# Kernel optimization log

Hardware: AMD Instinct MI355X
Metric: run time of the kernel (lower is better)

## Reference

```python
import jax, jax.numpy as jnp
import numpy as np
from jax import lax

LBDA = 0.5   # soft-min temperature from OTAM_cum_dist_v2 default
EPS = 0.01   # cos_sim epsilon


def otam_cum_dist(dists, lbda=LBDA):
    """Soft-DTW-style OTAM DP. dists: [nq, ns, L, S] -> [nq, ns].
    Faithful to OTAM_cum_dist_v2: pad last dim by (1,1) with zeros, then run the
    row-wise recurrence. Soft-min computed via stable logsumexp (same math as
    -lbda*log(sum exp(-x/lbda)))."""
    nq, ns, L, S = dists.shape
    d = jnp.pad(dists, ((0, 0), (0, 0), (0, 0), (1, 1)))  # [nq, ns, L, W], W=S+2
    W = S + 2
    # Row 0: cum[0, m] = cum[0, m-1] + d[0, m], cum[0, 0] = 0
    row0 = jnp.concatenate(
        [jnp.zeros((nq, ns, 1), d.dtype), jnp.cumsum(d[:, :, 0, 1:], axis=-1)], axis=-1)
    if L == 1:
        return row0[..., -1]

    m_idx = jnp.arange(1, W)
    include_up = (m_idx == 1) | (m_idx == W - 1)  # only first/last cols use cum[l-1, m]
    INF = jnp.asarray(jnp.inf, d.dtype)

    def row_step(prev_row, d_row):
        # prev_row, d_row: [nq, ns, W]
        xs = (
            jnp.moveaxis(d_row[:, :, 1:], -1, 0),        # d[l, m],       [W-1, nq, ns]
            jnp.moveaxis(prev_row[:, :, :-1], -1, 0),    # cum[l-1, m-1]
            jnp.moveaxis(prev_row[:, :, 1:], -1, 0),     # cum[l-1, m]
            include_up,
        )

        def col_step(cur_left, x):
            d_m, p_diag, p_up, inc = x
            up = jnp.where(inc, p_up, INF)               # masked term -> exp(-inf)=0
            terms = jnp.stack([p_diag, cur_left, up])    # [3, nq, ns]
            new = d_m - lbda * jax.nn.logsumexp(-terms / lbda, axis=0)
            return new, new

        _, cols = lax.scan(col_step, jnp.zeros((nq, ns), d.dtype), xs)
        row = jnp.concatenate(
            [jnp.zeros((nq, ns, 1), d.dtype), jnp.moveaxis(cols, 0, -1)], axis=-1)
        return row, None

    d_rows = jnp.moveaxis(d[:, :, 1:, :], 2, 0)          # [L-1, nq, ns, W]
    final_row, _ = lax.scan(row_step, row0, d_rows)
    return final_row[..., -1]


def reference(support_features, query_features):
    """OTAM meta-logits (cum_dist_g = -otam_distance) of DSN_TEMPORAL.
    support_features: [n_classes, L, D] class prototypes; query_features: [nq, L, D]."""
    nq, Lq, D = query_features.shape
    ns, Ls, _ = support_features.shape
    q = query_features.reshape(nq * Lq, D)
    s = support_features.reshape(ns * Ls, D)
    # cos_sim with epsilon in denominator (faithful to cos_sim())
    num = q @ s.T
    den = (jnp.linalg.norm(q, axis=-1)[:, None]
           * jnp.linalg.norm(s, axis=-1)[None, :] + EPS)
    frame_dists = 1.0 - num / den                         # [nq*L, ns*S]
    dists = frame_dists.reshape(nq, Lq, ns, Ls).transpose(0, 2, 1, 3)  # [nq, ns, L, S]
    cum = otam_cum_dist(dists) + otam_cum_dist(dists.transpose(0, 1, 3, 2))
    return -cum                                           # meta_logits [nq, ns]


def setup_inputs() -> dict:
    key = jax.random.key(0)
    k1, k2 = jax.random.split(key)
    return {
        "support_features": jax.random.normal(k1, (64, 8, 576), dtype=jnp.float32),
        "query_features": jax.random.normal(k2, (2048, 8, 576), dtype=jnp.float32),
    }
```

## Files before the change

### kernel.cpp

```cpp
#include <hip/hip_runtime.h>
#include <hip/hip_bf16.h>

#define D_K 576
#define NSLAB 18
#define LBDA_INV 2.0f
#define HALF_LBDA 0.5f
#define EPS 0.01f
#define DSTRIDE 136

typedef __attribute__((ext_vector_type(8))) short short8;
typedef __attribute__((ext_vector_type(4))) float f32x4;

__device__ inline float bf2f(unsigned short s) {
    return __uint_as_float(((unsigned)s) << 16);
}
__device__ inline unsigned pack_bf16(float x, float y) {
    __hip_bfloat162 h = __float22bfloat162_rn(float2{x, y});
    return *reinterpret_cast<unsigned*>(&h);
}

__device__ inline float softmin3(float a, float b, float c) {
    float mn = fminf(a, fminf(b, c));
    float s = __expf(-LBDA_INV * (a - mn)) + __expf(-LBDA_INV * (b - mn)) +
              __expf(-LBDA_INV * (c - mn));
    return mn - HALF_LBDA * __logf(s);
}
__device__ inline float softmin2(float a, float b) {
    float mn = fminf(a, b);
    float s = __expf(-LBDA_INV * (a - mn)) + __expf(-LBDA_INV * (b - mn));
    return mn - HALF_LBDA * __logf(s);
}

template <int RS, int CS>
__device__ float otam_dp(const float* d) {
    float prev[10], cur[10];
    prev[0] = 0.f;
#pragma unroll
    for (int m = 1; m <= 8; ++m) prev[m] = prev[m - 1] + d[0 * RS + (m - 1) * CS];
    prev[9] = prev[8];
#pragma unroll
    for (int l = 1; l < 8; ++l) {
        cur[0] = 0.f;
        cur[1] = d[l * RS + 0 * CS] + softmin3(prev[0], 0.f, prev[1]);
#pragma unroll
        for (int m = 2; m <= 8; ++m)
            cur[m] = d[l * RS + (m - 1) * CS] + softmin2(prev[m - 1], cur[m - 1]);
        cur[9] = softmin3(prev[8], cur[8], prev[9]);
#pragma unroll
        for (int m = 0; m < 10; ++m) prev[m] = cur[m];
    }
    return prev[9];
}

__global__ __launch_bounds__(256, 2) void fused_kernel(
        const float* __restrict__ sup, const float* __restrict__ qry,
        float* __restrict__ out) {
    __shared__ unsigned short smem[128 * DSTRIDE];
    __shared__ float qn_l[128], sn_l[128];
    unsigned short* As = smem;
    unsigned short* Bs = smem + 4096;
    unsigned short* Ds = smem;

    const int t = threadIdx.x;
    const int b = blockIdx.x;
    const int xcd = b & 7, s2 = b >> 3;
    const int sblk = s2 >> 4;
    const int qblk = xcd * 16 + (s2 & 15);

    const float* Ag = qry + (size_t)qblk * 128 * D_K;
    const float* Bg = sup + (size_t)sblk * 128 * D_K;

    const int lane = t & 63;
    const int wave = t >> 6;
    const int wm = wave >> 1, wn = wave & 1;
    const int col16 = lane & 15, quad = lane >> 4;

    f32x4 acc[4][4];
#pragma unroll
    for (int i = 0; i < 4; ++i)
#pragma unroll
        for (int j = 0; j < 4; ++j) acc[i][j] = (f32x4){0.f, 0.f, 0.f, 0.f};

    const int srow = t >> 3, scol = t & 7;
    const int c_in = scol >> 1, half = scol & 1;
    const int swz = c_in << 1;
    float sq_a[4] = {0.f, 0.f, 0.f, 0.f}, sq_b[4] = {0.f, 0.f, 0.f, 0.f};

    int aoff[4], boff[4];
#pragma unroll
    for (int mt = 0; mt < 4; ++mt) {
        int m = wm * 64 + mt * 16 + col16;
        aoff[mt] = (quad * 128 + (m ^ (quad << 1))) * 8;
    }
#pragma unroll
    for (int nt = 0; nt < 4; ++nt) {
        int n = wn * 64 + nt * 16 + col16;
        boff[nt] = (quad * 128 + (n ^ (quad << 1))) * 8;
    }

    for (int j = 0; j < NSLAB; ++j) {
        const int kbase = j * 32 + scol * 4;
        float4 va[4], vb[4];
#pragma unroll
        for (int i = 0; i < 4; ++i) {
            int r = i * 32 + srow;
            va[i] = *(const float4*)(Ag + (size_t)r * D_K + kbase);
            vb[i] = *(const float4*)(Bg + (size_t)r * D_K + kbase);
        }
#pragma unroll
        for (int i = 0; i < 4; ++i) {
            int r = i * 32 + srow;
            int off = (c_in * 128 + (r ^ swz)) * 8 + half * 4;
            sq_a[i] += va[i].x * va[i].x + va[i].y * va[i].y +
                       va[i].z * va[i].z + va[i].w * va[i].w;
            sq_b[i] += vb[i].x * vb[i].x + vb[i].y * vb[i].y +
                       vb[i].z * vb[i].z + vb[i].w * vb[i].w;
            *(uint2*)(As + off) = uint2{pack_bf16(va[i].x, va[i].y),
                                        pack_bf16(va[i].z, va[i].w)};
            *(uint2*)(Bs + off) = uint2{pack_bf16(vb[i].x, vb[i].y),
                                        pack_bf16(vb[i].z, vb[i].w)};
        }
        __syncthreads();

        short8 af[4], bf[4];
#pragma unroll
        for (int mt = 0; mt < 4; ++mt) af[mt] = *(const short8*)(As + aoff[mt]);
#pragma unroll
        for (int nt = 0; nt < 4; ++nt) bf[nt] = *(const short8*)(Bs + boff[nt]);
#pragma unroll
        for (int mt = 0; mt < 4; ++mt)
#pragma unroll
            for (int nt = 0; nt < 4; ++nt)
                acc[mt][nt] = __builtin_amdgcn_mfma_f32_16x16x32_bf16(
                    af[mt], bf[nt], acc[mt][nt], 0, 0, 0);
        __syncthreads();
    }

#pragma unroll
    for (int i = 0; i < 4; ++i) {
        sq_a[i] += __shfl_down(sq_a[i], 4);
        sq_a[i] += __shfl_down(sq_a[i], 2);
        sq_a[i] += __shfl_down(sq_a[i], 1);
        sq_b[i] += __shfl_down(sq_b[i], 4);
        sq_b[i] += __shfl_down(sq_b[i], 2);
        sq_b[i] += __shfl_down(sq_b[i], 1);
    }
    if ((t & 7) == 0) {
        int r = t >> 3;
#pragma unroll
        for (int i = 0; i < 4; ++i) {
            qn_l[i * 32 + r] = sqrtf(sq_a[i]);
            sn_l[i * 32 + r] = sqrtf(sq_b[i]);
        }
    }
    __syncthreads();

#pragma unroll
    for (int mt = 0; mt < 4; ++mt) {
#pragma unroll
        for (int reg = 0; reg < 4; ++reg) {
            int m = wm * 64 + mt * 16 + quad * 4 + reg;
            float qv = qn_l[m];
#pragma unroll
            for (int nt = 0; nt < 4; ++nt) {
                int n = wn * 64 + nt * 16 + col16;
                float sv = sn_l[n];
                float dist = 1.f - acc[mt][nt][reg] / (qv * sv + EPS);
                unsigned p = pack_bf16(dist, 0.f);
                Ds[m * DSTRIDE + n] = (unsigned short)(p & 0xFFFF);
            }
        }
    }
    __syncthreads();

    const int ql = t >> 4, sl = t & 15;
    float d[64];
#pragma unroll
    for (int l = 0; l < 8; ++l) {
        short8 rowv = *(const short8*)(&Ds[(ql * 8 + l) * DSTRIDE + sl * 8]);
#pragma unroll
        for (int jj = 0; jj < 8; ++jj) d[l * 8 + jj] = bf2f((unsigned short)rowv[jj]);
    }
    float r1 = otam_dp<8, 1>(d);
    float r2 = otam_dp<1, 8>(d);
    int qg = qblk * 16 + ql, sg = sblk * 16 + sl;
    out[qg * 64 + sg] = -(r1 + r2);
}

extern "C" void kernel_launch(void* const* d_in, const int* in_sizes, int n_in,
                              void* d_out, int out_size, void* d_ws, size_t ws_size,
                              hipStream_t stream) {
    const float* sup = (const float*)d_in[0];
    const float* qry = (const float*)d_in[1];
    float* out = (float*)d_out;
    fused_kernel<<<dim3(512), dim3(256), 0, stream>>>(sup, qry, out);
}
```

Measured before the change: 126.1 us.

## Retile fused GEMM+DP to 64x256 blocks with per-wave column split

Changes each block's tile from 128 query rows × 128 support rows to 64 query rows × 256 support rows. All four waves now share the same A rows and each wave owns a 64-column slice of B. The grid mapping drops the XCD-aware swizzle for a simple qblk/shalf split. Support data is reloaded by only two block halves, but each block now loads 2x more B per slab (8 float4 per thread versus 2 for A). This changes the global load mix and register pressure, and the output writes now cover 8 queries by 32 supports per block.

```diff
diff --git a/kernel.cpp b/kernel.cpp
--- a/kernel.cpp
+++ b/kernel.cpp
@@ -6,7 +6,7 @@
 #define LBDA_INV 2.0f
 #define HALF_LBDA 0.5f
 #define EPS 0.01f
-#define DSTRIDE 136
+#define DST 264
 
 typedef __attribute__((ext_vector_type(8))) short short8;
 typedef __attribute__((ext_vector_type(4))) float f32x4;
@@ -55,24 +55,22 @@
 __global__ __launch_bounds__(256, 2) void fused_kernel(
         const float* __restrict__ sup, const float* __restrict__ qry,
         float* __restrict__ out) {
-    __shared__ unsigned short smem[128 * DSTRIDE];
-    __shared__ float qn_l[128], sn_l[128];
+    __shared__ unsigned short smem[64 * DST];
+    __shared__ float qn_l[64], sn_l[256];
     unsigned short* As = smem;
-    unsigned short* Bs = smem + 4096;
+    unsigned short* Bs = smem + 2048;
     unsigned short* Ds = smem;
 
     const int t = threadIdx.x;
     const int b = blockIdx.x;
-    const int xcd = b & 7, s2 = b >> 3;
-    const int sblk = s2 >> 4;
-    const int qblk = xcd * 16 + (s2 & 15);
-
-    const float* Ag = qry + (size_t)qblk * 128 * D_K;
-    const float* Bg = sup + (size_t)sblk * 128 * D_K;
+    const int shalf = b >> 8;
+    const int qblk = b & 255;
+
+    const float* Ag = qry + (size_t)qblk * 64 * D_K;
+    const float* Bg = sup + (size_t)shalf * 256 * D_K;
 
     const int lane = t & 63;
     const int wave = t >> 6;
-    const int wm = wave >> 1, wn = wave & 1;
     const int col16 = lane & 15, quad = lane >> 4;
 
     f32x4 acc[4][4];
@@ -82,41 +80,46 @@
         for (int j = 0; j < 4; ++j) acc[i][j] = (f32x4){0.f, 0.f, 0.f, 0.f};
 
     const int srow = t >> 3, scol = t & 7;
-    const int c_in = scol >> 1, half = scol & 1;
-    const int swz = c_in << 1;
-    float sq_a[4] = {0.f, 0.f, 0.f, 0.f}, sq_b[4] = {0.f, 0.f, 0.f, 0.f};
+    const int c_in = scol >> 1, half = scol & 1, swz = c_in << 1;
+    float sq_a[2] = {0.f, 0.f};
+    float sq_b[8] = {0.f, 0.f, 0.f, 0.f, 0.f, 0.f, 0.f, 0.f};
 
     int aoff[4], boff[4];
 #pragma unroll
     for (int mt = 0; mt < 4; ++mt) {
-        int m = wm * 64 + mt * 16 + col16;
-        aoff[mt] = (quad * 128 + (m ^ (quad << 1))) * 8;
+        int m = mt * 16 + col16;
+        aoff[mt] = (quad * 64 + (m ^ (quad << 1))) * 8;
     }
 #pragma unroll
     for (int nt = 0; nt < 4; ++nt) {
-        int n = wn * 64 + nt * 16 + col16;
-        boff[nt] = (quad * 128 + (n ^ (quad << 1))) * 8;
+        int n = wave * 64 + nt * 16 + col16;
+        boff[nt] = (quad * 256 + (n ^ (quad << 1))) * 8;
     }
 
     for (int j = 0; j < NSLAB; ++j) {
         const int kbase = j * 32 + scol * 4;
-        float4 va[4], vb[4];
-#pragma unroll
-        for (int i = 0; i < 4; ++i) {
+        float4 va[2], vb[8];
+#pragma unroll
+        for (int i = 0; i < 2; ++i)
+            va[i] = *(const float4*)(Ag + (size_t)(i * 32 + srow) * D_K + kbase);
+#pragma unroll
+        for (int i = 0; i < 8; ++i)
+            vb[i] = *(const float4*)(Bg + (size_t)(i * 32 + srow) * D_K + kbase);
+#pragma unroll
+        for (int i = 0; i < 2; ++i) {
             int r = i * 32 + srow;
-            va[i] = *(const float4*)(Ag + (size_t)r * D_K + kbase);
-            vb[i] = *(const float4*)(Bg + (size_t)r * D_K + kbase);
-        }
-#pragma unroll
-        for (int i = 0; i < 4; ++i) {
-            int r = i * 32 + srow;
-            int off = (c_in * 128 + (r ^ swz)) * 8 + half * 4;
             sq_a[i] += va[i].x * va[i].x + va[i].y * va[i].y +
                        va[i].z * va[i].z + va[i].w * va[i].w;
+            int off = (c_in * 64 + (r ^ swz)) * 8 + half * 4;
+            *(uint2*)(As + off) = uint2{pack_bf16(va[i].x, va[i].y),
+                                        pack_bf16(va[i].z, va[i].w)};
+        }
+#pragma unroll
+        for (int i = 0; i < 8; ++i) {
+            int r = i * 32 + srow;
             sq_b[i] += vb[i].x * vb[i].x + vb[i].y * vb[i].y +
                        vb[i].z * vb[i].z + vb[i].w * vb[i].w;
-            *(uint2*)(As + off) = uint2{pack_bf16(va[i].x, va[i].y),
-                                        pack_bf16(va[i].z, va[i].w)};
+            int off = (c_in * 256 + (r ^ swz)) * 8 + half * 4;
             *(uint2*)(Bs + off) = uint2{pack_bf16(vb[i].x, vb[i].y),
                                         pack_bf16(vb[i].z, vb[i].w)};
         }
@@ -137,21 +140,22 @@
     }
 
 #pragma unroll
-    for (int i = 0; i < 4; ++i) {
+    for (int i = 0; i < 2; ++i) {
         sq_a[i] += __shfl_down(sq_a[i], 4);
         sq_a[i] += __shfl_down(sq_a[i], 2);
         sq_a[i] += __shfl_down(sq_a[i], 1);
+    }
+#pragma unroll
+    for (int i = 0; i < 8; ++i) {
         sq_b[i] += __shfl_down(sq_b[i], 4);
         sq_b[i] += __shfl_down(sq_b[i], 2);
         sq_b[i] += __shfl_down(sq_b[i], 1);
     }
     if ((t & 7) == 0) {
-        int r = t >> 3;
-#pragma unroll
-        for (int i = 0; i < 4; ++i) {
-            qn_l[i * 32 + r] = sqrtf(sq_a[i]);
-            sn_l[i * 32 + r] = sqrtf(sq_b[i]);
-        }
+#pragma unroll
+        for (int i = 0; i < 2; ++i) qn_l[i * 32 + srow] = sqrtf(sq_a[i]);
+#pragma unroll
+        for (int i = 0; i < 8; ++i) sn_l[i * 32 + srow] = sqrtf(sq_b[i]);
     }
     __syncthreads();
 
@@ -159,31 +163,31 @@
     for (int mt = 0; mt < 4; ++mt) {
 #pragma unroll
         for (int reg = 0; reg < 4; ++reg) {
-            int m = wm * 64 + mt * 16 + quad * 4 + reg;
+            int m = mt * 16 + quad * 4 + reg;
             float qv = qn_l[m];
 #pragma unroll
             for (int nt = 0; nt < 4; ++nt) {
-                int n = wn * 64 + nt * 16 + col16;
+                int n = wave * 64 + nt * 16 + col16;
                 float sv = sn_l[n];
                 float dist = 1.f - acc[mt][nt][reg] / (qv * sv + EPS);
                 unsigned p = pack_bf16(dist, 0.f);
-                Ds[m * DSTRIDE + n] = (unsigned short)(p & 0xFFFF);
+                Ds[m * DST + n] = (unsigned short)(p & 0xFFFF);
             }
         }
     }
     __syncthreads();
 
-    const int ql = t >> 4, sl = t & 15;
+    const int ql = t >> 5, sl = t & 31;
     float d[64];
 #pragma unroll
     for (int l = 0; l < 8; ++l) {
-        short8 rowv = *(const short8*)(&Ds[(ql * 8 + l) * DSTRIDE + sl * 8]);
+        short8 rowv = *(const short8*)(&Ds[(ql * 8 + l) * DST + sl * 8]);
 #pragma unroll
         for (int jj = 0; jj < 8; ++jj) d[l * 8 + jj] = bf2f((unsigned short)rowv[jj]);
     }
     float r1 = otam_dp<8, 1>(d);
     float r2 = otam_dp<1, 8>(d);
-    int qg = qblk * 16 + ql, sg = sblk * 16 + sl;
+    int qg = qblk * 8 + ql, sg = shalf * 32 + sl;
     out[qg * 64 + sg] = -(r1 + r2);
 }
 
```

After: 136.4 us. +8.2%, slower.
